# Optimization experiments

Hardware: AMD Instinct MI355X
Metric: run time of the kernel (lower is better)

Reference implementation:

```python
import jax, jax.numpy as jnp
import numpy as np

B, L, V, E, D, NH, HD, NL = 4, 2048, 32000, 300, 128, 4, 128, 3
D2 = NH * HD  # 512
W = 3  # ring window size (unfold_size)
EPS = 1e-5


def setup_inputs() -> dict:
    key = jax.random.key(0)
    ks = jax.random.split(key, 16)
    s = 0.02
    w = lambda k, shape: (jax.random.normal(k, shape, jnp.float32) * s)
    inp = {
        "tokens": jax.random.randint(ks[0], (B, L), 0, V),
        "mask": jax.random.randint(ks[1], (B, L), 0, 2).astype(jnp.int32),
        "emb_table": w(ks[2], (V, E)),
        "proj_w": w(ks[3], (D, E)),
        "proj_b": jnp.zeros((D,), jnp.float32),
        "ng": jnp.ones((NL, D), jnp.float32),
        "nb": jnp.zeros((NL, D), jnp.float32),
        "rq_w": w(ks[4], (NL, D2, D)), "rq_b": jnp.zeros((NL, D2), jnp.float32),
        "rk_w": w(ks[5], (NL, D2, D)), "rk_b": jnp.zeros((NL, D2), jnp.float32),
        "rv_w": w(ks[6], (NL, D2, D)), "rv_b": jnp.zeros((NL, D2), jnp.float32),
        "ro_w": w(ks[7], (NL, D, D2)), "ro_b": jnp.zeros((NL, D), jnp.float32),
        "sq_w": w(ks[8], (NL, D2, D)), "sq_b": jnp.zeros((NL, D2), jnp.float32),
        "sk_w": w(ks[9], (NL, D2, D)), "sk_b": jnp.zeros((NL, D2), jnp.float32),
        "sv_w": w(ks[10], (NL, D2, D)), "sv_b": jnp.zeros((NL, D2), jnp.float32),
        "so_w": w(ks[11], (NL, D, D2)), "so_b": jnp.zeros((NL, D), jnp.float32),
    }
    return inp


def _layernorm(x, g, b):
    mu = x.mean(-1, keepdims=True)
    var = x.var(-1, keepdims=True)
    return (x - mu) / jnp.sqrt(var + EPS) * g + b


def reference(tokens, mask, emb_table, proj_w, proj_b, ng, nb,
              rq_w, rq_b, rk_w, rk_b, rv_w, rv_b, ro_w, ro_b,
              sq_w, sq_b, sk_w, sk_b, sv_w, sv_b, so_w, so_b):
    b, l = tokens.shape
    pad = (mask == 0)                                        # [B,L] True at padding
    smask = jnp.concatenate([jnp.zeros((b, 1), bool), pad], axis=1)  # [B,L+1]
    x = emb_table[tokens] @ proj_w.T + proj_b                # [B,L,D]
    nodes = x
    relay = x.mean(axis=1)                                   # [B,D]
    r_embs = x                                               # fixed original embeddings
    scale = 1.0 / np.sqrt(HD).astype(np.float32)
    for i in range(NL):
        nx = _layernorm(nodes, ng[i], nb[i])
        # ----- MSA1: ring (windowed) attention + relay extras -----
        q = (nx @ rq_w[i].T + rq_b[i]).reshape(b, l, NH, HD)
        k = (nx @ rk_w[i].T + rk_b[i]).reshape(b, l, NH, HD)
        v = (nx @ rv_w[i].T + rv_b[i]).reshape(b, l, NH, HD)
        relay_bc = jnp.broadcast_to(relay[:, None, :], (b, l, D))
        ax = jnp.stack([r_embs, relay_bc], axis=2)           # [B,L,2,D]
        ak = (ax @ rk_w[i].T + rk_b[i]).reshape(b, l, 2, NH, HD)
        av = (ax @ rv_w[i].T + rv_b[i]).reshape(b, l, 2, NH, HD)
        kp = jnp.pad(k, ((0, 0), (1, 1), (0, 0), (0, 0)))    # zero pad like F.unfold
        vp = jnp.pad(v, ((0, 0), (1, 1), (0, 0), (0, 0)))
        kw = jnp.stack([kp[:, u:u + l] for u in range(W)], axis=2)  # [B,L,3,NH,HD]
        vw = jnp.stack([vp[:, u:u + l] for u in range(W)], axis=2)
        kall = jnp.concatenate([kw, ak], axis=2)             # [B,L,5,NH,HD]
        vall = jnp.concatenate([vw, av], axis=2)
        scores = jnp.einsum('blnh,blunh->blun', q, kall) * scale
        alphas = jax.nn.softmax(scores, axis=2)
        att = jnp.einsum('blun,blunh->blnh', alphas, vall).reshape(b, l, D2)
        nodes = nodes + jax.nn.leaky_relu(att @ ro_w[i].T + ro_b[i])
        # ----- MSA2: relay (global) attention over [relay; nodes] -----
        y = jnp.concatenate([relay[:, None, :], nodes], axis=1)      # [B,L+1,D]
        sq = (relay @ sq_w[i].T + sq_b[i]).reshape(b, NH, HD)
        sk = (y @ sk_w[i].T + sk_b[i]).reshape(b, l + 1, NH, HD)
        sv = (y @ sv_w[i].T + sv_b[i]).reshape(b, l + 1, NH, HD)
        pre = jnp.einsum('bnh,blnh->bnl', sq, sk) * scale            # [B,NH,L+1]
        pre = jnp.where(smask[:, None, :], -jnp.inf, pre)
        al = jax.nn.softmax(pre, axis=2)
        satt = jnp.einsum('bnl,blnh->bnh', al, sv).reshape(b, D2)
        relay = jax.nn.leaky_relu(satt @ so_w[i].T + so_b[i])
        nodes = jnp.where(pad[:, :, None], 0.0, nodes)
    return relay  # a_v: [B, d_model] (use_attention=False path)
```

## Files before the change

kernel.cpp:

```cpp
#include <hip/hip_runtime.h>
#include <hip/hip_bf16.h>

constexpr int B = 4, L = 2048, E = 300, D = 128, NH = 4, HD = 128, NL = 3, D2 = 512;
constexpr float EPS = 1e-5f;
constexpr float SCALE = 0.08838834764831843f;
constexpr int NCH = 64;

typedef unsigned int uint_t;
typedef unsigned short u16;
typedef short bf16x8 __attribute__((ext_vector_type(8)));
typedef float f32x4 __attribute__((ext_vector_type(4)));

__device__ __forceinline__ u16 f2bf(float f) {
  union { float f; uint_t i; } x; x.f = f;
  uint_t r = x.i + 0x7fffu + ((x.i >> 16) & 1u);
  return (u16)(r >> 16);
}
__device__ __forceinline__ uint_t packbf(float a, float b) {
  return (uint_t)f2bf(a) | ((uint_t)f2bf(b) << 16);
}
__device__ __forceinline__ float2 bf2x2(uint_t u) {
  union { uint_t i; float f; } a, b;
  a.i = (u & 0xffffu) << 16; b.i = u & 0xffff0000u;
  return make_float2(a.f, b.f);
}
struct f8 { float v[8]; };
__device__ __forceinline__ f8 unpack8(uint4 u) {
  f8 r;
  float2 a = bf2x2(u.x); r.v[0] = a.x; r.v[1] = a.y;
  float2 b = bf2x2(u.y); r.v[2] = b.x; r.v[3] = b.y;
  float2 c = bf2x2(u.z); r.v[4] = c.x; r.v[5] = c.y;
  float2 d = bf2x2(u.w); r.v[6] = d.x; r.v[7] = d.y;
  return r;
}

struct WCArgs { const float* s[4]; u16* d[4]; };
__global__ __launch_bounds__(256) void wconv(WCArgs wa) {
  int ti = blockIdx.y;
  const float* s = wa.s[ti]; u16* dd = wa.d[ti];
  int i = (blockIdx.x * 256 + threadIdx.x) * 4;
  float4 f = *(const float4*)(s + i);
  *(uint2*)(dd + i) = make_uint2(packbf(f.x, f.y), packbf(f.z, f.w));
}

struct GDesc { const u16* A; const u16* W; const float* bias; u16* outb; };
struct GArgs { GDesc d[5]; };
struct PArgs {
  int mode;
  const float* rel_in;
  const float* pm; const float* ps; const float* pw;
  const float* uprev; const float* cvprev;
  const float* svw; const float* svb;
  const float* sow; const float* sob;
  float* rel_out;
  const float* rkw; const float* rkb;
  const float* rvw; const float* rvb;
  const float* sqw; const float* sqb;
  const float* skw; const float* skb;
  float* relay_k; float* relay_v;
  float* u; float* cvec;
};
constexpr int NPROJ = 24;

__global__ __launch_bounds__(256) void gemm_qkv(GArgs ga, PArgs pa, int N) {
  int bid = blockIdx.x;
  int t = threadIdx.x;
  if (bid < NPROJ) {
    __shared__ float rel[D];
    __shared__ float sql2[2][HD];
    __shared__ float credp[4];
    __shared__ float wsum2[NH][D];
    __shared__ float satts[D2];
    __shared__ float ecs2[256];
    int b = bid / 6, j = bid % 6;
    int wv = t >> 6, lane = t & 63;
    if (pa.mode) {
      if (t < D) rel[t] = pa.rel_in[(size_t)b * D + t];
      __syncthreads();
      float2 uu = ((const float2*)(pa.uprev + ((size_t)b * NH + wv) * D))[lane];
      float2 rr = ((const float2*)rel)[lane];
      float pdot = uu.x * rr.x + uu.y * rr.y;
#pragma unroll
      for (int o = 1; o < 64; o <<= 1) pdot += __shfl_xor(pdot, o, 64);
      float s0 = pdot + pa.cvprev[b * NH + wv];
      int bn = b * NH + wv;
      float pmv = pa.pm[bn * NCH + lane];
      float m = fmaxf(pmv, s0);
#pragma unroll
      for (int o = 1; o < 64; o <<= 1) m = fmaxf(m, __shfl_xor(m, o, 64));
      float ec = expf(pmv - m);
      ecs2[wv * 64 + lane] = ec;
      float sc = pa.ps[bn * NCH + lane] * ec;
#pragma unroll
      for (int o = 1; o < 64; o <<= 1) sc += __shfl_xor(sc, o, 64);
      float e0 = expf(s0 - m);
      float invS = 1.0f / (e0 + sc);
      float2 a;
      a.x = e0 * rel[lane * 2]; a.y = e0 * rel[lane * 2 + 1];
      const float* pwb = pa.pw + (size_t)bn * NCH * D;
#pragma unroll 8
      for (int c = 0; c < NCH; c++) {
        float2 pw2 = ((const float2*)(pwb + (size_t)c * D))[lane];
        float e = ecs2[wv * 64 + c];
        a.x += e * pw2.x; a.y += e * pw2.y;
      }
      wsum2[wv][lane * 2] = a.x * invS;
      wsum2[wv][lane * 2 + 1] = a.y * invS;
      __syncthreads();
#pragma unroll
      for (int pp = 0; pp < 2; pp++) {
        int nh = pp * 256 + t, n = nh >> 7;
        float acc = pa.svb[nh];
        const float4* wp = (const float4*)(pa.svw + (size_t)nh * D);
        const float4* wl = (const float4*)wsum2[n];
#pragma unroll 8
        for (int dd = 0; dd < D / 4; dd++) {
          float4 x = wl[dd], y = wp[dd];
          acc += x.x * y.x + x.y * y.y + x.z * y.z + x.w * y.w;
        }
        satts[nh] = acc;
      }
      __syncthreads();
      {
        int part = t >> 7, col = t & 127;
        float acc = 0.f;
        const float4* wp = (const float4*)(pa.sow + (size_t)col * D2 + part * 256);
        const float4* a4 = (const float4*)(satts + part * 256);
#pragma unroll 8
        for (int jj = 0; jj < 64; jj++) {
          float4 x = a4[jj], y = wp[jj];
          acc += x.x * y.x + x.y * y.y + x.z * y.z + x.w * y.w;
        }
        ecs2[part * 128 + col] = acc;
      }
      __syncthreads();
      if (t < D) {
        float av = pa.sob[t] + ecs2[t] + ecs2[128 + t];
        av = (av > 0.f) ? av : 0.01f * av;
        rel[t] = av;
        pa.rel_out[(size_t)b * D + t] = av;
      }
      __syncthreads();
    } else {
      if (t < D) rel[t] = pa.rel_in[(size_t)b * D + t];
      __syncthreads();
    }
    const float4* r4 = (const float4*)rel;
    if (j < 4) {
      int which = j >> 1;
      int n = (j & 1) * 256 + t;
      const float* W = which ? pa.rvw : pa.rkw;
      float acc = (which ? pa.rvb : pa.rkb)[n];
      const float4* w4 = (const float4*)(W + (size_t)n * D);
#pragma unroll 8
      for (int i = 0; i < D / 4; i++) {
        float4 w = w4[i], r = r4[i];
        acc += w.x * r.x + w.y * r.y + w.z * r.z + w.w * r.w;
      }
      (which ? pa.relay_v : pa.relay_k)[(size_t)b * D2 + n] = acc;
    } else {
      int hh = t >> 7, th = t & 127;
      int n = (j - 4) * 2 + hh;
      int nh = n * HD + th;
      float acc = pa.sqb[nh];
      const float4* w4 = (const float4*)(pa.sqw + (size_t)nh * D);
#pragma unroll 8
      for (int i = 0; i < D / 4; i++) {
        float4 w = w4[i], r = r4[i];
        acc += w.x * r.x + w.y * r.y + w.z * r.z + w.w * r.w;
      }
      sql2[hh][th] = acc;
      __syncthreads();
      float cp = acc * pa.skb[nh];
#pragma unroll
      for (int o = 1; o < 64; o <<= 1) cp += __shfl_xor(cp, o, 64);
      if ((t & 63) == 0) credp[t >> 6] = cp;
      float a0 = 0.f, a1 = 0.f, a2 = 0.f, a3 = 0.f;
      const float* wp = pa.skw + (size_t)(n * HD) * D + th;
      for (int hx = 0; hx < HD; hx += 4) {
        a0 += sql2[hh][hx] * wp[(size_t)hx * D];
        a1 += sql2[hh][hx + 1] * wp[(size_t)(hx + 1) * D];
        a2 += sql2[hh][hx + 2] * wp[(size_t)(hx + 2) * D];
        a3 += sql2[hh][hx + 3] * wp[(size_t)(hx + 3) * D];
      }
      pa.u[((size_t)b * NH + n) * D + th] = (a0 + a1 + a2 + a3) * SCALE;
      __syncthreads();
      if (th == 0) pa.cvec[b * NH + n] = (credp[2 * hh] + credp[2 * hh + 1]) * SCALE;
    }
    return;
  }
  __shared__ u16 As[128][136];
  __shared__ u16 Ws[128][136];
  int g = bid - NPROJ;
  int bm = g & 63;
  int y = g >> 6;
  int di = y >> 2, bn = y & 3;
  GDesc d = ga.d[di];
  const int rowA = bm * 128, rowW = bn * 128;

  f32x4 acc[4][4];
#pragma unroll
  for (int i = 0; i < 4; i++)
#pragma unroll
    for (int j = 0; j < 4; j++)
      acc[i][j] = (f32x4){0.f, 0.f, 0.f, 0.f};

  const int r = t >> 1, c0 = (t & 1) * 64;
  const int wid = t >> 6;
  const int wm = (wid & 1) * 64, wn = (wid >> 1) * 64;
  const int lr = t & 15, quad = (t >> 4) & 3;

  const u16* Arow = d.A + (size_t)(rowA + r) * 128;
  const u16* Wrow = d.W + (size_t)(rowW + r) * 128;
  uint4 av_[8], wv_[8];
#pragma unroll
  for (int i = 0; i < 8; i++) {
    av_[i] = *(const uint4*)(Arow + c0 + i * 8);
    wv_[i] = *(const uint4*)(Wrow + c0 + i * 8);
  }
#pragma unroll
  for (int i = 0; i < 8; i++) {
    *(uint4*)&As[r][c0 + i * 8] = av_[i];
    *(uint4*)&Ws[r][c0 + i * 8] = wv_[i];
  }
  __syncthreads();
#pragma unroll
  for (int ks = 0; ks < 4; ks++) {
    bf16x8 af[4], bfr[4];
#pragma unroll
    for (int mt = 0; mt < 4; mt++)
      af[mt] = *(const bf16x8*)&As[wm + mt * 16 + lr][ks * 32 + quad * 8];
#pragma unroll
    for (int nt = 0; nt < 4; nt++)
      bfr[nt] = *(const bf16x8*)&Ws[wn + nt * 16 + lr][ks * 32 + quad * 8];
#pragma unroll
    for (int mt = 0; mt < 4; mt++)
#pragma unroll
      for (int nt = 0; nt < 4; nt++)
        acc[mt][nt] = __builtin_amdgcn_mfma_f32_16x16x32_bf16(af[mt], bfr[nt], acc[mt][nt], 0, 0, 0);
  }
  __syncthreads();
#pragma unroll
  for (int nt = 0; nt < 4; nt++) {
    int colL = wn + nt * 16 + lr;
    float bv = d.bias[rowW + colL];
#pragma unroll
    for (int mt = 0; mt < 4; mt++) {
#pragma unroll
      for (int rr = 0; rr < 4; rr++) {
        int rowL = wm + mt * 16 + quad * 4 + rr;
        As[rowL][colL] = f2bf(acc[mt][nt][rr] + bv);
      }
    }
  }
  __syncthreads();
#pragma unroll
  for (int rep = 0; rep < 8; rep++) {
    int lin = rep * 256 + t;
    int rowL = lin >> 4, colL = (lin & 15) * 8;
    uint4 v = *(const uint4*)&As[rowL][colL];
    *(uint4*)&d.outb[(size_t)(rowA + rowL) * N + rowW + colL] = v;
  }
}

__global__ __launch_bounds__(256) void gemm_embed_ln(
    const float* __restrict__ emb, const float* __restrict__ W,
    const float* __restrict__ bias, const int* __restrict__ gather,
    const float* __restrict__ lng, const float* __restrict__ lnb,
    float* __restrict__ nodes, u16* __restrict__ xb, u16* __restrict__ nxb,
    float* __restrict__ relay) {
  __shared__ u16 As[64][72];
  __shared__ u16 Ws[128][72];
  __shared__ float C[64][132];
  __shared__ float gb[2][D];
  __shared__ float lmu[64], lrs[64];
  int t = threadIdx.x;
  int bm = blockIdx.x;
  const int rowA0 = bm * 64;

  f32x4 acc[2][4];
#pragma unroll
  for (int i = 0; i < 2; i++)
#pragma unroll
    for (int j = 0; j < 4; j++)
      acc[i][j] = (f32x4){0.f, 0.f, 0.f, 0.f};

  const int wid = t >> 6;
  const int wm = (wid & 1) * 32, wn = (wid >> 1) * 64;
  const int lr = t & 15, quad = (t >> 4) & 3;
  const int ra = t >> 2, ca = (t & 3) * 16;
  const int rw = t >> 1, cw = (t & 1) * 32;

  if (t < D) { gb[0][t] = lng[t]; gb[1][t] = lnb[t]; }

  const float* Arow = emb + (size_t)gather[rowA0 + ra] * E;
  const float* Wrow = W + (size_t)rw * E;

  for (int kt = 0; kt < E; kt += 64) {
    __syncthreads();
    bool full = (kt + 64 <= E);
#pragma unroll
    for (int ch = 0; ch < 4; ch++) {
      int c = kt + ca + ch * 4;
      float4 fa;
      if (full) fa = *(const float4*)(Arow + c);
      else {
        fa.x = (c + 0 < E) ? Arow[c + 0] : 0.f;
        fa.y = (c + 1 < E) ? Arow[c + 1] : 0.f;
        fa.z = (c + 2 < E) ? Arow[c + 2] : 0.f;
        fa.w = (c + 3 < E) ? Arow[c + 3] : 0.f;
      }
      *(uint2*)&As[ra][ca + ch * 4] = make_uint2(packbf(fa.x, fa.y), packbf(fa.z, fa.w));
    }
#pragma unroll
    for (int ch = 0; ch < 8; ch++) {
      int c = kt + cw + ch * 4;
      float4 fw;
      if (full) fw = *(const float4*)(Wrow + c);
      else {
        fw.x = (c + 0 < E) ? Wrow[c + 0] : 0.f;
        fw.y = (c + 1 < E) ? Wrow[c + 1] : 0.f;
        fw.z = (c + 2 < E) ? Wrow[c + 2] : 0.f;
        fw.w = (c + 3 < E) ? Wrow[c + 3] : 0.f;
      }
      *(uint2*)&Ws[rw][cw + ch * 4] = make_uint2(packbf(fw.x, fw.y), packbf(fw.z, fw.w));
    }
    __syncthreads();
#pragma unroll
    for (int ks = 0; ks < 2; ks++) {
      bf16x8 af[2], bfr[4];
#pragma unroll
      for (int mt = 0; mt < 2; mt++)
        af[mt] = *(const bf16x8*)&As[wm + mt * 16 + lr][ks * 32 + quad * 8];
#pragma unroll
      for (int nt = 0; nt < 4; nt++)
        bfr[nt] = *(const bf16x8*)&Ws[wn + nt * 16 + lr][ks * 32 + quad * 8];
#pragma unroll
      for (int mt = 0; mt < 2; mt++)
#pragma unroll
        for (int nt = 0; nt < 4; nt++)
          acc[mt][nt] = __builtin_amdgcn_mfma_f32_16x16x32_bf16(af[mt], bfr[nt], acc[mt][nt], 0, 0, 0);
    }
  }
#pragma unroll
  for (int nt = 0; nt < 4; nt++) {
    int col = wn + nt * 16 + lr;
    float bv = bias[col];
#pragma unroll
    for (int mt = 0; mt < 2; mt++) {
#pragma unroll
      for (int rr = 0; rr < 4; rr++) {
        int row = wm + mt * 16 + quad * 4 + rr;
        C[row][col] = acc[mt][nt][rr] + bv;
      }
    }
  }
  __syncthreads();
  if (t < 64) {
    float s = 0.f, s2 = 0.f;
#pragma unroll 16
    for (int j = 0; j < D; j++) { float v = C[t][j]; s += v; s2 += v * v; }
    float mu = s * (1.0f / D);
    float var = s2 * (1.0f / D) - mu * mu;
    lmu[t] = mu; lrs[t] = rsqrtf(var + EPS);
  }
  __syncthreads();
#pragma unroll
  for (int rep = 0; rep < 8; rep++) {
    int lin = rep * 1024 + t * 4;
    int row = lin >> 7, col = lin & 127;
    float4 v = *(const float4*)&C[row][col];
    size_t g = (size_t)(rowA0 + row) * D + col;
    *(float4*)&nodes[g] = v;
    *(uint2*)&xb[g] = make_uint2(packbf(v.x, v.y), packbf(v.z, v.w));
    float mu = lmu[row], rs = lrs[row];
    float o0 = (v.x - mu) * rs * gb[0][col] + gb[1][col];
    float o1 = (v.y - mu) * rs * gb[0][col + 1] + gb[1][col + 1];
    float o2 = (v.z - mu) * rs * gb[0][col + 2] + gb[1][col + 2];
    float o3 = (v.w - mu) * rs * gb[0][col + 3] + gb[1][col + 3];
    *(uint2*)&nxb[g] = make_uint2(packbf(o0, o1), packbf(o2, o3));
  }
  if (t < D) {
    int b = rowA0 >> 11;
    float s = 0.f;
#pragma unroll 16
    for (int r2 = 0; r2 < 64; r2++) s += C[r2][t];
    atomicAdd(&relay[b * D + t], s * (1.0f / L));
  }
}

__global__ __launch_bounds__(512) void attn_ro_ln(
    const u16* __restrict__ q, const u16* __restrict__ k, const u16* __restrict__ v,
    const u16* __restrict__ akr, const u16* __restrict__ avr,
    const float* __restrict__ rkvec, const float* __restrict__ rvvec,
    const u16* __restrict__ W,
    const float* __restrict__ bias,
    const int* __restrict__ mask,
    const float* __restrict__ lng, const float* __restrict__ lnb,
    const float* __restrict__ uvec, const float* __restrict__ cvec,
    float* __restrict__ nodes, u16* __restrict__ nxb,
    float* __restrict__ pm, float* __restrict__ ps, float* __restrict__ pw,
    int do_ln) {
  __shared__ u16 att[32][520];
  __shared__ u16 Ws[128][136];
  __shared__ float C[32][132];
  __shared__ float gb[2][D];
  __shared__ float lmu[32], lrs[32];
  __shared__ float usv[NH][D];
  __shared__ float cv2[NH];
  __shared__ float scs[NH][32];
  __shared__ float esr[NH][32];
  int t = threadIdx.x;
  int bm = blockIdx.x;
  const int rowA0 = bm * 32;
  const int b4 = rowA0 >> 11;
  const int chunk = (rowA0 >> 5) & 63;
  const int wid = t >> 6, lane = t & 63;

  if (do_ln && t < D) { gb[0][t] = lng[t]; gb[1][t] = lnb[t]; }
  usv[t >> 7][t & 127] = uvec[(size_t)b4 * NH * D + t];
  if (t < NH) cv2[t] = cvec[b4 * NH + t];

  {
    size_t rb = (size_t)b4 * D2 + lane * 8;
    float4 rk0 = *(const float4*)(rkvec + rb), rk1 = *(const float4*)(rkvec + rb + 4);
    float4 rv0 = *(const float4*)(rvvec + rb), rv1 = *(const float4*)(rvvec + rb + 4);
    f8 krel, vrel;
    krel.v[0] = rk0.x; krel.v[1] = rk0.y; krel.v[2] = rk0.z; krel.v[3] = rk0.w;
    krel.v[4] = rk1.x; krel.v[5] = rk1.y; krel.v[6] = rk1.z; krel.v[7] = rk1.w;
    vrel.v[0] = rv0.x; vrel.v[1] = rv0.y; vrel.v[2] = rv0.z; vrel.v[3] = rv0.w;
    vrel.v[4] = rv1.x; vrel.v[5] = rv1.y; vrel.v[6] = rv1.z; vrel.v[7] = rv1.w;
#pragma unroll
    for (int i = 0; i < 4; i++) {
      int rr_ = wid * 4 + i;
      int gr = rowA0 + rr_;
      int l = gr & (L - 1);
      size_t rowoff = (size_t)gr * D2 + lane * 8;
      uint4 qd = *(const uint4*)(q + rowoff);
      uint4 kd[4], vd[4];
#pragma unroll
      for (int u2 = 0; u2 < 3; u2++) {
        int ll = l + u2 - 1;
        bool ok = (ll >= 0 && ll < L);
        size_t off = rowoff + (size_t)(u2 - 1) * (size_t)D2;
        if (ok) { kd[u2] = *(const uint4*)(k + off); vd[u2] = *(const uint4*)(v + off); }
        else { kd[u2] = make_uint4(0, 0, 0, 0); vd[u2] = make_uint4(0, 0, 0, 0); }
      }
      kd[3] = *(const uint4*)(akr + rowoff);
      vd[3] = *(const uint4*)(avr + rowoff);
      f8 qf = unpack8(qd);
      f8 kf[5], vf[5];
#pragma unroll
      for (int u2 = 0; u2 < 4; u2++) { kf[u2] = unpack8(kd[u2]); vf[u2] = unpack8(vd[u2]); }
      kf[4] = krel; vf[4] = vrel;
      float s[5];
#pragma unroll
      for (int u2 = 0; u2 < 5; u2++) {
        float p = 0.f;
#pragma unroll
        for (int j = 0; j < 8; j++) p += qf.v[j] * kf[u2].v[j];
#pragma unroll
        for (int o = 1; o < 16; o <<= 1) p += __shfl_xor(p, o, 64);
        s[u2] = p * SCALE;
      }
      float m = s[0];
#pragma unroll
      for (int u2 = 1; u2 < 5; u2++) m = fmaxf(m, s[u2]);
      float e[5], sum = 0.f;
#pragma unroll
      for (int u2 = 0; u2 < 5; u2++) { e[u2] = expf(s[u2] - m); sum += e[u2]; }
      float inv = 1.0f / sum;
      float o8[8];
#pragma unroll
      for (int j = 0; j < 8; j++) {
        float a = 0.f;
#pragma unroll
        for (int u2 = 0; u2 < 5; u2++) a += e[u2] * vf[u2].v[j];
        o8[j] = a * inv;
      }
      uint4 od;
      od.x = packbf(o8[0], o8[1]); od.y = packbf(o8[2], o8[3]);
      od.z = packbf(o8[4], o8[5]); od.w = packbf(o8[6], o8[7]);
      *(uint4*)&att[rr_][lane * 8] = od;
    }
  }
  __syncthreads();

  f32x4 acc[2];
  acc[0] = (f32x4){0.f, 0.f, 0.f, 0.f};
  acc[1] = (f32x4){0.f, 0.f, 0.f, 0.f};
  const int wm = (wid & 1) * 16, wn = (wid >> 1) * 32;
  const int lr = t & 15, quad = (t >> 4) & 3;
  const int rw = t >> 2, cw = (t & 3) * 32;
  const u16* Wrow = W + (size_t)rw * 512;
  for (int kt = 0; kt < 512; kt += 128) {
    uint4 w0 = *(const uint4*)(Wrow + kt + cw);
    uint4 w1 = *(const uint4*)(Wrow + kt + cw + 8);
    uint4 w2 = *(const uint4*)(Wrow + kt + cw + 16);
    uint4 w3 = *(const uint4*)(Wrow + kt + cw + 24);
    __syncthreads();
    *(uint4*)&Ws[rw][cw] = w0; *(uint4*)&Ws[rw][cw + 8] = w1;
    *(uint4*)&Ws[rw][cw + 16] = w2; *(uint4*)&Ws[rw][cw + 24] = w3;
    __syncthreads();
#pragma unroll
    for (int ks = 0; ks < 4; ks++) {
      bf16x8 af = *(const bf16x8*)&att[wm + lr][kt + ks * 32 + quad * 8];
#pragma unroll
      for (int nt = 0; nt < 2; nt++) {
        bf16x8 bfr = *(const bf16x8*)&Ws[wn + nt * 16 + lr][ks * 32 + quad * 8];
        acc[nt] = __builtin_amdgcn_mfma_f32_16x16x32_bf16(af, bfr, acc[nt], 0, 0, 0);
      }
    }
  }
  __syncthreads();
#pragma unroll
  for (int nt = 0; nt < 2; nt++) {
    int col = wn + nt * 16 + lr;
    float bv = bias[col];
#pragma unroll
    for (int rr = 0; rr < 4; rr++) {
      int row = wm + quad * 4 + rr;
      float vv = acc[nt][rr] + bv;
      vv = (vv > 0.f) ? vv : 0.01f * vv;
      vv += nodes[(size_t)(rowA0 + row) * D + col];
      if (mask[rowA0 + row] == 0) vv = 0.f;
      C[row][col] = vv;
    }
  }
  __syncthreads();
  if (t < 32) {
    float s = 0.f, s2 = 0.f;
#pragma unroll 16
    for (int j = 0; j < D; j++) { float vv = C[t][j]; s += vv; s2 += vv * vv; }
    float mu = s * (1.0f / D);
    float var = s2 * (1.0f / D) - mu * mu;
    lmu[t] = mu; lrs[t] = rsqrtf(var + EPS);
  }
  __syncthreads();
#pragma unroll
  for (int rep = 0; rep < 2; rep++) {
    int lin = rep * 2048 + t * 4;
    int row = lin >> 7, col = lin & 127;
    float4 vv = *(const float4*)&C[row][col];
    size_t g = (size_t)(rowA0 + row) * D + col;
    *(float4*)&nodes[g] = vv;
    if (do_ln) {
      float mu = lmu[row], rs = lrs[row];
      float o0 = (vv.x - mu) * rs * gb[0][col] + gb[1][col];
      float o1 = (vv.y - mu) * rs * gb[0][col + 1] + gb[1][col + 1];
      float o2 = (vv.z - mu) * rs * gb[0][col + 2] + gb[1][col + 2];
      float o3 = (vv.w - mu) * rs * gb[0][col + 3] + gb[1][col + 3];
      *(uint2*)&nxb[g] = make_uint2(packbf(o0, o1), packbf(o2, o3));
    }
  }
  if (wid < 4) {
    int n = wid;
    int bn = b4 * NH + n;
    const float2* un = (const float2*)usv[n];
    float2 uv2 = un[lane];
    for (int r2 = 0; r2 < 32; r2++) {
      float2 cc = ((const float2*)&C[r2][0])[lane];
      float p = uv2.x * cc.x + uv2.y * cc.y;
#pragma unroll
      for (int o = 1; o < 64; o <<= 1) p += __shfl_xor(p, o, 64);
      if (lane == 0) {
        float s = p + cv2[n];
        if (mask[rowA0 + r2] == 0) s = -1e30f;
        scs[n][r2] = s;
      }
    }
    float m = -1e30f;
    for (int r2 = 0; r2 < 32; r2++) m = fmaxf(m, scs[n][r2]);
    if (lane < 32) esr[n][lane] = expf(scs[n][lane] - m);
    float sum = 0.f;
    for (int r2 = 0; r2 < 32; r2++) sum += esr[n][r2];
    if (lane == 0) { pm[bn * NCH + chunk] = m; ps[bn * NCH + chunk] = sum; }
    float a0 = 0.f, a1 = 0.f;
    for (int r2 = 0; r2 < 32; r2++) {
      float e = esr[n][r2];
      float2 cc = ((const float2*)&C[r2][0])[lane];
      a0 += e * cc.x; a1 += e * cc.y;
    }
    float* pwp = pw + ((size_t)bn * NCH + chunk) * D + 2 * lane;
    pwp[0] = a0; pwp[1] = a1;
  }
}

__global__ __launch_bounds__(512) void relay_combine(
    const float* __restrict__ pm, const float* __restrict__ ps,
    const float* __restrict__ pw,
    const float* __restrict__ relay_entry,
    const float* __restrict__ uvec_in, const float* __restrict__ cvec_in,
    const float* __restrict__ svw, const float* __restrict__ svb,
    const float* __restrict__ sow, const float* __restrict__ sob,
    float* __restrict__ relay_out) {
  __shared__ float rel0[D];
  __shared__ float wpart[8];
  __shared__ float ecs[NH][NCH];
  __shared__ float wsum[NH][D];
  __shared__ float satts[D2];
  __shared__ float rred[4][D];
  int b = blockIdx.x, t = threadIdx.x;
  int n = t >> 7, h = t & 127;
  int w = t >> 6, lane = t & 63;
  if (t < D) rel0[t] = relay_entry[(size_t)b * D + t];
  __syncthreads();
  float p = uvec_in[((size_t)b * NH + n) * D + h] * rel0[h];
#pragma unroll
  for (int o = 1; o < 64; o <<= 1) p += __shfl_xor(p, o, 64);
  if (lane == 0) wpart[w] = p;
  __syncthreads();
  float s0 = wpart[2 * n] + wpart[2 * n + 1] + cvec_in[b * NH + n];
  int c = h & 63;
  float pmv = pm[(b * NH + n) * NCH + c];
  float m = fmaxf(pmv, s0);
#pragma unroll
  for (int o = 1; o < 64; o <<= 1) m = fmaxf(m, __shfl_xor(m, o, 64));
  float ec = expf(pmv - m);
  if (h < 64) ecs[n][h] = ec;
  float sc = ps[(b * NH + n) * NCH + c] * ec;
#pragma unroll
  for (int o = 1; o < 64; o <<= 1) sc += __shfl_xor(sc, o, 64);
  float e0 = expf(s0 - m);
  float invS = 1.0f / (e0 + sc);
  __syncthreads();
  float acc = e0 * rel0[h];
  const float* pwp = pw + ((size_t)(b * NH + n) * NCH) * D + h;
#pragma unroll 8
  for (int cc = 0; cc < NCH; cc++) acc += ecs[n][cc] * pwp[(size_t)cc * D];
  wsum[n][h] = acc * invS;
  __syncthreads();
  {
    float a = svb[t];
    const float4* wp = (const float4*)(svw + (size_t)t * D);
    const float4* wl = (const float4*)wsum[n];
#pragma unroll 8
    for (int dd = 0; dd < D / 4; dd++) {
      float4 x = wl[dd], y = wp[dd];
      a += x.x * y.x + x.y * y.y + x.z * y.z + x.w * y.w;
    }
    satts[t] = a;
  }
  __syncthreads();
  {
    int part = t >> 7, col = t & 127;
    float a = 0.f;
    const float4* wp = (const float4*)(sow + (size_t)col * D2 + part * 128);
    const float4* a4 = (const float4*)(satts + part * 128);
#pragma unroll 8
    for (int jj = 0; jj < 32; jj++) {
      float4 x = a4[jj], y = wp[jj];
      a += x.x * y.x + x.y * y.y + x.z * y.z + x.w * y.w;
    }
    rred[part][col] = a;
  }
  __syncthreads();
  if (t < D) {
    float a = sob[t] + rred[0][t] + rred[1][t] + rred[2][t] + rred[3][t];
    a = (a > 0.f) ? a : 0.01f * a;
    relay_out[(size_t)b * D + t] = a;
  }
}

extern "C" void kernel_launch(void* const* d_in, const int* in_sizes, int n_in,
                              void* d_out, int out_size, void* d_ws, size_t ws_size,
                              hipStream_t stream) {
  const int* tokens = (const int*)d_in[0];
  const int* mask = (const int*)d_in[1];
  const float* emb = (const float*)d_in[2];
  const float* proj_w = (const float*)d_in[3];
  const float* proj_b = (const float*)d_in[4];
  const float* ng = (const float*)d_in[5];
  const float* nb = (const float*)d_in[6];
  const float* rq_w = (const float*)d_in[7], * rq_b = (const float*)d_in[8];
  const float* rk_w = (const float*)d_in[9], * rk_b = (const float*)d_in[10];
  const float* rv_w = (const float*)d_in[11], * rv_b = (const float*)d_in[12];
  const float* ro_w = (const float*)d_in[13], * ro_b = (const float*)d_in[14];
  const float* sq_w = (const float*)d_in[15], * sq_b = (const float*)d_in[16];
  const float* sk_w = (const float*)d_in[17], * sk_b = (const float*)d_in[18];
  const float* sv_w = (const float*)d_in[19], * sv_b = (const float*)d_in[20];
  const float* so_w = (const float*)d_in[21], * so_b = (const float*)d_in[22];

  const size_t BLD = (size_t)B * L * D;
  const size_t BLD4 = (size_t)B * L * D2;
  const size_t WTEN = (size_t)NL * D * D2;

  float* fp = (float*)d_ws;
  float* nodes = fp;                    fp += BLD;
  float* rbuf0 = fp;                    fp += B * D;
  float* rbuf1 = fp;                    fp += B * D;
  float* relay_k = fp;                  fp += B * D2;
  float* relay_v = fp;                  fp += B * D2;
  float* uv0 = fp;                      fp += B * NH * D;
  float* uv1 = fp;                      fp += B * NH * D;
  float* cv0 = fp;                      fp += B * NH;
  float* cv1 = fp;                      fp += B * NH;
  float* pm = fp;                       fp += B * NH * NCH;
  float* ps = fp;                       fp += B * NH * NCH;
  float* pw = fp;                       fp += (size_t)B * NH * NCH * D;
  u16* up = (u16*)fp;
  u16* xb = up;                         up += BLD;
  u16* nxb = up;                        up += BLD;
  u16* qb = up;                         up += BLD4;
  u16* kb = up;                         up += BLD4;
  u16* vb = up;                         up += BLD4;
  u16* akb = up;                        up += BLD4;
  u16* avb = up;                        up += BLD4;
  u16* wb = up;
  u16* wrq = wb, * wrk = wb + WTEN, * wrv = wb + 2 * WTEN, * wro = wb + 3 * WTEN;

  float* uv[2] = {uv0, uv1};
  float* cv[2] = {cv0, cv1};

  hipMemsetAsync(rbuf0, 0, B * D * sizeof(float), stream);

  {
    WCArgs wa;
    wa.s[0] = rq_w; wa.s[1] = rk_w; wa.s[2] = rv_w; wa.s[3] = ro_w;
    wa.d[0] = wrq; wa.d[1] = wrk; wa.d[2] = wrv; wa.d[3] = wro;
    wconv<<<dim3(WTEN / 1024, 4), 256, 0, stream>>>(wa);
  }
  gemm_embed_ln<<<128, 256, 0, stream>>>(emb, proj_w, proj_b, tokens, ng, nb,
                                         nodes, xb, nxb, rbuf0);

  float* rel_in_l[3] = {rbuf0, rbuf0, rbuf1};
  float* rel_out_l[3] = {nullptr, rbuf1, rbuf0};

  for (int i = 0; i < NL; i++) {
    const size_t wo = (size_t)i * D * D2;
    const float* rqbi = rq_b + (size_t)i * D2;
    const float* rkbi = rk_b + (size_t)i * D2;
    const float* rvbi = rv_b + (size_t)i * D2;
    const float* robi = ro_b + (size_t)i * D;
    const int e = i & 1, ep = (i > 0) ? ((i - 1) & 1) : 0;
    const int last = (i == NL - 1);

    {
      GArgs ga = {};
      ga.d[0] = {nxb, wrq + wo, rqbi, qb};
      ga.d[1] = {nxb, wrk + wo, rkbi, kb};
      ga.d[2] = {nxb, wrv + wo, rvbi, vb};
      ga.d[3] = {xb,  wrk + wo, rkbi, akb};
      ga.d[4] = {xb,  wrv + wo, rvbi, avb};
      PArgs pa;
      pa.mode = (i == 0) ? 0 : 1;
      pa.rel_in = rel_in_l[i];
      pa.pm = pm; pa.ps = ps; pa.pw = pw;
      pa.uprev = uv[ep]; pa.cvprev = cv[ep];
      const size_t wprev = (size_t)(i > 0 ? i - 1 : 0) * D * D2;
      pa.svw = sv_w + wprev; pa.svb = sv_b + (size_t)(i > 0 ? i - 1 : 0) * D2;
      pa.sow = so_w + wprev; pa.sob = so_b + (size_t)(i > 0 ? i - 1 : 0) * D;
      pa.rel_out = rel_out_l[i];
      pa.rkw = rk_w + wo; pa.rkb = rkbi;
      pa.rvw = rv_w + wo; pa.rvb = rvbi;
      pa.sqw = sq_w + wo; pa.sqb = sq_b + (size_t)i * D2;
      pa.skw = sk_w + wo; pa.skb = sk_b + (size_t)i * D2;
      pa.relay_k = relay_k; pa.relay_v = relay_v; pa.u = uv[e]; pa.cvec = cv[e];
      gemm_qkv<<<64 * 20 + NPROJ, 256, 0, stream>>>(ga, pa, D2);
    }
    attn_ro_ln<<<256, 512, 0, stream>>>(
        qb, kb, vb, akb, avb, relay_k, relay_v,
        wro + wo, robi, mask,
        last ? nullptr : ng + (i + 1) * D, last ? nullptr : nb + (i + 1) * D,
        uv[e], cv[e], nodes, nxb, pm, ps, pw, last ? 0 : 1);
  }
  const size_t w2 = (size_t)(NL - 1) * D * D2;
  relay_combine<<<B, 512, 0, stream>>>(pm, ps, pw, rbuf0,
                                       uv[(NL - 1) & 1], cv[(NL - 1) & 1],
                                       sv_w + w2, sv_b + (size_t)(NL - 1) * D2,
                                       so_w + w2, so_b + (size_t)(NL - 1) * D,
                                       (float*)d_out);
}
```

Measured before the change: 319.7 us.

## Reuse A tile across QKV outputs, fuse weight conversion, drop LDS staging

The QKV GEMM now loads each 128-row activation tile into shared memory once and loops over the three (or two) weight tensors that share it. This cuts the launch from 1280 to 512 tiles and removes redundant A loads, but each block now runs several GEMMs back to back. The fp32-to-bf16 weight conversion is folded into the embedding kernel as extra blocks, which saves one launch. The output projection in attn_ro_ln reads weight fragments straight from global memory instead of staging them in shared memory, which drops barriers and LDS use at the cost of uncoalesced global reads.

```diff
diff --git a/kernel.cpp b/kernel.cpp
--- a/kernel.cpp
+++ b/kernel.cpp
@@ -35,13 +35,6 @@
 }
 
 struct WCArgs { const float* s[4]; u16* d[4]; };
-__global__ __launch_bounds__(256) void wconv(WCArgs wa) {
-  int ti = blockIdx.y;
-  const float* s = wa.s[ti]; u16* dd = wa.d[ti];
-  int i = (blockIdx.x * 256 + threadIdx.x) * 4;
-  float4 f = *(const float4*)(s + i);
-  *(uint2*)(dd + i) = make_uint2(packbf(f.x, f.y), packbf(f.z, f.w));
-}
 
 struct GDesc { const u16* A; const u16* W; const float* bias; u16* outb; };
 struct GArgs { GDesc d[5]; };
@@ -192,90 +185,107 @@
   __shared__ u16 As[128][136];
   __shared__ u16 Ws[128][136];
   int g = bid - NPROJ;
-  int bm = g & 63;
-  int y = g >> 6;
-  int di = y >> 2, bn = y & 3;
-  GDesc d = ga.d[di];
+  int grp = g >> 8;
+  int bm = (g & 255) >> 2, bn = g & 3;
+  const int di0 = grp ? 3 : 0;
+  const int ntens = grp ? 2 : 3;
   const int rowA = bm * 128, rowW = bn * 128;
-
-  f32x4 acc[4][4];
-#pragma unroll
-  for (int i = 0; i < 4; i++)
-#pragma unroll
-    for (int j = 0; j < 4; j++)
-      acc[i][j] = (f32x4){0.f, 0.f, 0.f, 0.f};
 
   const int r = t >> 1, c0 = (t & 1) * 64;
   const int wid = t >> 6;
   const int wm = (wid & 1) * 64, wn = (wid >> 1) * 64;
   const int lr = t & 15, quad = (t >> 4) & 3;
 
-  const u16* Arow = d.A + (size_t)(rowA + r) * 128;
-  const u16* Wrow = d.W + (size_t)(rowW + r) * 128;
-  uint4 av_[8], wv_[8];
-#pragma unroll
-  for (int i = 0; i < 8; i++) {
-    av_[i] = *(const uint4*)(Arow + c0 + i * 8);
-    wv_[i] = *(const uint4*)(Wrow + c0 + i * 8);
-  }
-#pragma unroll
-  for (int i = 0; i < 8; i++) {
-    *(uint4*)&As[r][c0 + i * 8] = av_[i];
-    *(uint4*)&Ws[r][c0 + i * 8] = wv_[i];
-  }
-  __syncthreads();
-#pragma unroll
-  for (int ks = 0; ks < 4; ks++) {
-    bf16x8 af[4], bfr[4];
-#pragma unroll
-    for (int mt = 0; mt < 4; mt++)
-      af[mt] = *(const bf16x8*)&As[wm + mt * 16 + lr][ks * 32 + quad * 8];
-#pragma unroll
-    for (int nt = 0; nt < 4; nt++)
-      bfr[nt] = *(const bf16x8*)&Ws[wn + nt * 16 + lr][ks * 32 + quad * 8];
-#pragma unroll
-    for (int mt = 0; mt < 4; mt++)
+  {
+    const u16* Arow = ga.d[di0].A + (size_t)(rowA + r) * 128;
+    uint4 av_[8];
+#pragma unroll
+    for (int i = 0; i < 8; i++) av_[i] = *(const uint4*)(Arow + c0 + i * 8);
+#pragma unroll
+    for (int i = 0; i < 8; i++) *(uint4*)&As[r][c0 + i * 8] = av_[i];
+  }
+  for (int ti = 0; ti < ntens; ti++) {
+    GDesc d = ga.d[di0 + ti];
+    {
+      const u16* Wrow = d.W + (size_t)(rowW + r) * 128;
+      uint4 wv_[8];
+#pragma unroll
+      for (int i = 0; i < 8; i++) wv_[i] = *(const uint4*)(Wrow + c0 + i * 8);
+#pragma unroll
+      for (int i = 0; i < 8; i++) *(uint4*)&Ws[r][c0 + i * 8] = wv_[i];
+    }
+    __syncthreads();
+    f32x4 acc[4][4];
+#pragma unroll
+    for (int i = 0; i < 4; i++)
+#pragma unroll
+      for (int j = 0; j < 4; j++)
+        acc[i][j] = (f32x4){0.f, 0.f, 0.f, 0.f};
+#pragma unroll
+    for (int ks = 0; ks < 4; ks++) {
+      bf16x8 af[4], bfr[4];
+#pragma unroll
+      for (int mt = 0; mt < 4; mt++)
+        af[mt] = *(const bf16x8*)&As[wm + mt * 16 + lr][ks * 32 + quad * 8];
 #pragma unroll
       for (int nt = 0; nt < 4; nt++)
-        acc[mt][nt] = __builtin_amdgcn_mfma_f32_16x16x32_bf16(af[mt], bfr[nt], acc[mt][nt], 0, 0, 0);
-  }
-  __syncthreads();
-#pragma unroll
-  for (int nt = 0; nt < 4; nt++) {
-    int colL = wn + nt * 16 + lr;
-    float bv = d.bias[rowW + colL];
-#pragma unroll
-    for (int mt = 0; mt < 4; mt++) {
-#pragma unroll
-      for (int rr = 0; rr < 4; rr++) {
-        int rowL = wm + mt * 16 + quad * 4 + rr;
-        As[rowL][colL] = f2bf(acc[mt][nt][rr] + bv);
-      }
-    }
-  }
-  __syncthreads();
-#pragma unroll
-  for (int rep = 0; rep < 8; rep++) {
-    int lin = rep * 256 + t;
-    int rowL = lin >> 4, colL = (lin & 15) * 8;
-    uint4 v = *(const uint4*)&As[rowL][colL];
-    *(uint4*)&d.outb[(size_t)(rowA + rowL) * N + rowW + colL] = v;
+        bfr[nt] = *(const bf16x8*)&Ws[wn + nt * 16 + lr][ks * 32 + quad * 8];
+#pragma unroll
+      for (int mt = 0; mt < 4; mt++)
+#pragma unroll
+        for (int nt = 0; nt < 4; nt++)
+          acc[mt][nt] = __builtin_amdgcn_mfma_f32_16x16x32_bf16(af[mt], bfr[nt], acc[mt][nt], 0, 0, 0);
+    }
+    __syncthreads();
+#pragma unroll
+    for (int nt = 0; nt < 4; nt++) {
+      int colL = wn + nt * 16 + lr;
+      float bv = d.bias[rowW + colL];
+#pragma unroll
+      for (int mt = 0; mt < 4; mt++) {
+#pragma unroll
+        for (int rr = 0; rr < 4; rr++) {
+          int rowL = wm + mt * 16 + quad * 4 + rr;
+          Ws[rowL][colL] = f2bf(acc[mt][nt][rr] + bv);
+        }
+      }
+    }
+    __syncthreads();
+#pragma unroll
+    for (int rep = 0; rep < 8; rep++) {
+      int lin = rep * 256 + t;
+      int rowL = lin >> 4, colL = (lin & 15) * 8;
+      uint4 v = *(const uint4*)&Ws[rowL][colL];
+      *(uint4*)&d.outb[(size_t)(rowA + rowL) * N + rowW + colL] = v;
+    }
+    __syncthreads();
   }
 }
 
 __global__ __launch_bounds__(256) void gemm_embed_ln(
+    WCArgs wa,
     const float* __restrict__ emb, const float* __restrict__ W,
     const float* __restrict__ bias, const int* __restrict__ gather,
     const float* __restrict__ lng, const float* __restrict__ lnb,
     float* __restrict__ nodes, u16* __restrict__ xb, u16* __restrict__ nxb,
     float* __restrict__ relay) {
+  int bid = blockIdx.x;
+  int t = threadIdx.x;
+  if (bid >= 128) {
+    int cb = bid - 128;
+    int ti = cb / 192, xi = cb - ti * 192;
+    const float* s = wa.s[ti]; u16* dd = wa.d[ti];
+    int i = (xi * 256 + t) * 4;
+    float4 f = *(const float4*)(s + i);
+    *(uint2*)(dd + i) = make_uint2(packbf(f.x, f.y), packbf(f.z, f.w));
+    return;
+  }
   __shared__ u16 As[64][72];
   __shared__ u16 Ws[128][72];
   __shared__ float C[64][132];
   __shared__ float gb[2][D];
   __shared__ float lmu[64], lrs[64];
-  int t = threadIdx.x;
-  int bm = blockIdx.x;
+  int bm = bid;
   const int rowA0 = bm * 64;
 
   f32x4 acc[2][4];
@@ -402,7 +412,6 @@
     float* __restrict__ pm, float* __restrict__ ps, float* __restrict__ pw,
     int do_ln) {
   __shared__ u16 att[32][520];
-  __shared__ u16 Ws[128][136];
   __shared__ float C[32][132];
   __shared__ float gb[2][D];
   __shared__ float lmu[32], lrs[32];
@@ -491,28 +500,18 @@
   acc[1] = (f32x4){0.f, 0.f, 0.f, 0.f};
   const int wm = (wid & 1) * 16, wn = (wid >> 1) * 32;
   const int lr = t & 15, quad = (t >> 4) & 3;
-  const int rw = t >> 2, cw = (t & 3) * 32;
-  const u16* Wrow = W + (size_t)rw * 512;
+#pragma unroll
   for (int kt = 0; kt < 512; kt += 128) {
-    uint4 w0 = *(const uint4*)(Wrow + kt + cw);
-    uint4 w1 = *(const uint4*)(Wrow + kt + cw + 8);
-    uint4 w2 = *(const uint4*)(Wrow + kt + cw + 16);
-    uint4 w3 = *(const uint4*)(Wrow + kt + cw + 24);
-    __syncthreads();
-    *(uint4*)&Ws[rw][cw] = w0; *(uint4*)&Ws[rw][cw + 8] = w1;
-    *(uint4*)&Ws[rw][cw + 16] = w2; *(uint4*)&Ws[rw][cw + 24] = w3;
-    __syncthreads();
 #pragma unroll
     for (int ks = 0; ks < 4; ks++) {
       bf16x8 af = *(const bf16x8*)&att[wm + lr][kt + ks * 32 + quad * 8];
 #pragma unroll
       for (int nt = 0; nt < 2; nt++) {
-        bf16x8 bfr = *(const bf16x8*)&Ws[wn + nt * 16 + lr][ks * 32 + quad * 8];
+        bf16x8 bfr = *(const bf16x8*)(W + (size_t)(wn + nt * 16 + lr) * 512 + kt + ks * 32 + quad * 8);
         acc[nt] = __builtin_amdgcn_mfma_f32_16x16x32_bf16(af, bfr, acc[nt], 0, 0, 0);
       }
     }
   }
-  __syncthreads();
 #pragma unroll
   for (int nt = 0; nt < 2; nt++) {
     int col = wn + nt * 16 + lr;
@@ -718,10 +717,9 @@
     WCArgs wa;
     wa.s[0] = rq_w; wa.s[1] = rk_w; wa.s[2] = rv_w; wa.s[3] = ro_w;
     wa.d[0] = wrq; wa.d[1] = wrk; wa.d[2] = wrv; wa.d[3] = wro;
-    wconv<<<dim3(WTEN / 1024, 4), 256, 0, stream>>>(wa);
-  }
-  gemm_embed_ln<<<128, 256, 0, stream>>>(emb, proj_w, proj_b, tokens, ng, nb,
-                                         nodes, xb, nxb, rbuf0);
+    gemm_embed_ln<<<128 + 768, 256, 0, stream>>>(wa, emb, proj_w, proj_b, tokens,
+                                                 ng, nb, nodes, xb, nxb, rbuf0);
+  }
 
   float* rel_in_l[3] = {rbuf0, rbuf0, rbuf1};
   float* rel_out_l[3] = {nullptr, rbuf1, rbuf0};
@@ -756,7 +754,7 @@
       pa.sqw = sq_w + wo; pa.sqb = sq_b + (size_t)i * D2;
       pa.skw = sk_w + wo; pa.skb = sk_b + (size_t)i * D2;
       pa.relay_k = relay_k; pa.relay_v = relay_v; pa.u = uv[e]; pa.cvec = cv[e];
-      gemm_qkv<<<64 * 20 + NPROJ, 256, 0, stream>>>(ga, pa, D2);
+      gemm_qkv<<<512 + NPROJ, 256, 0, stream>>>(ga, pa, D2);
     }
     attn_ro_ln<<<256, 512, 0, stream>>>(
         qb, kb, vb, akb, avb, relay_k, relay_v,
```

New measurement: 335.3 us. +4.9%, slower.
